# Kernel optimization log

Measured on AMD Instinct MI355X. Metric: run time of the kernel, lower is better.

## Reference

```python
import jax, jax.numpy as jnp
import numpy as np

N, F, H, C = 2048, 64, 64, 8

def setup_inputs() -> dict:
    key = jax.random.key(0)
    ks = jax.random.split(key, 8)
    s = 0.05  # small init like xavier gain=0.01
    return {
        "x": jax.random.normal(ks[0], (N, F), jnp.float32),
        "node_distances": jax.random.uniform(ks[1], (N, N), jnp.float32),
        "normalization_matrix": jnp.ones((N, N), jnp.float32),
        "W1": jax.random.normal(ks[2], (F, H), jnp.float32) * s,
        "b1": jnp.zeros((F, H), jnp.float32),
        "W2": jax.random.normal(ks[3], (F, H, C), jnp.float32) * s,
        "b2": jnp.zeros((F, C), jnp.float32),
        "Wm1": jax.random.normal(ks[4], (H,), jnp.float32) * s,
        "bm1": jnp.zeros((H,), jnp.float32),
        "Wm2": jax.random.normal(ks[5], (H,), jnp.float32) * s,
        "bm2": jnp.zeros((), jnp.float32),
    }

def reference(x, node_distances, normalization_matrix, W1, b1, W2, b2, Wm1, bm1, Wm2, bm2):
    # Per-feature NAM MLPs, vectorized over all F features (input dim is 1).
    # h[n,f,:] = relu(x[n,f] * W1[f] + b1[f])
    h = jax.nn.relu(x[:, :, None] * W1[None, :, :] + b1[None, :, :])        # [N,F,H]
    fx = jnp.einsum('nfh,fhc->nfc', h, W2) + b2[None, :, :]                 # [N,F,C]
    # Distance MLP m: Linear(1,H)->ReLU->Linear(H,1), limited_m => scalar weight per pair.
    d = node_distances / normalization_matrix                               # [N,N]
    hm = jax.nn.relu(d[:, :, None] * Wm1 + bm1)                             # [N,N,H]
    m = hm @ Wm2 + bm2                                                      # [N,N]
    # mf[c,i,f] = sum_j m[i,j]*fx[j,f,c]; out[c,i] = sum_f mf[c,i,f]
    # => out[i,c] = sum_j m[i,j] * (sum_f fx[j,f,c])  (identical math, fused)
    g = fx.sum(axis=1)                                                      # [N,C]
    out = m @ g                                                             # [N,C] == torch out.T
    return out
```

## Files before the change

kernel.cpp:

```cpp
#include <hip/hip_runtime.h>

#define NN 2048
#define FF 64
#define HH 64
#define CC 8
#define NB 2

#define INF __builtin_inff()

#define WS_T 0
#define WS_A 64
#define WS_B 129
#define WS_G 256

__global__ __launch_bounds__(256) void fused1_kernel(
    const float* __restrict__ x, const float* __restrict__ W1,
    const float* __restrict__ b1, const float* __restrict__ W2,
    const float* __restrict__ b2,
    const float* __restrict__ Wm1, const float* __restrict__ bm1,
    const float* __restrict__ Wm2, const float* __restrict__ bm2,
    float* __restrict__ ws)
{
    if (blockIdx.x == 256) {
        if (threadIdx.x >= 64) return;
        const int lane = threadIdx.x;

        float w  = Wm1[lane];
        float b  = bm1[lane];
        float m2 = Wm2[lane];
        float th = (w != 0.f) ? (-b / w) : INF;

        float v = th;
#pragma unroll
        for (int k = 2; k <= 64; k <<= 1) {
#pragma unroll
            for (int j = k >> 1; j >= 1; j >>= 1) {
                float o = __shfl_xor(v, j);
                bool up = ((lane & k) == 0);
                bool lower = ((lane & j) == 0);
                float mn = fminf(v, o), mx = fmaxf(v, o);
                v = (up == lower) ? mn : mx;
            }
        }
        ws[WS_T + lane] = v;

        float lo  = __shfl_up(v, 1);
        float hi  = v;
        float t63 = __shfl(v, 63);

        float dt;
        if (lane == 0) dt = (hi == INF) ? 0.f : hi - 1.f;
        else if (hi == INF) dt = (lo == INF) ? INF : lo + 1.f;
        else dt = 0.5f * (lo + hi);
        float dt64 = (t63 == INF) ? INF : t63 + 1.f;

        const float bm2v = bm2[0];
        float alpha = 0.f, beta = bm2v;
        float a64 = 0.f, b64 = bm2v;
#pragma unroll 8
        for (int h = 0; h < HH; ++h) {
            float wh = __shfl(w, h);
            float bh = __shfl(b, h);
            float mh = __shfl(m2, h);
            float tt = __shfl(th, h);
            bool act = (wh > 0.f) ? (dt > tt)
                     : ((wh < 0.f) ? (dt < tt) : (bh > 0.f));
            if (act) { alpha = fmaf(mh, wh, alpha); beta = fmaf(mh, bh, beta); }
            bool act64 = (wh > 0.f) ? (dt64 > tt)
                       : ((wh < 0.f) ? (dt64 < tt) : (bh > 0.f));
            if (act64) { a64 = fmaf(mh, wh, a64); b64 = fmaf(mh, bh, b64); }
        }
        ws[WS_A + lane] = alpha;
        ws[WS_B + lane] = beta;
        if (lane == 0) { ws[WS_A + 64] = a64; ws[WS_B + 64] = b64; }
        return;
    }

    float* g = ws + WS_G;
    const int wave = (blockIdx.x * 256 + threadIdx.x) >> 6;
    const int lane = threadIdx.x & 63;
    const int n0 = wave * NB;

    float xr[NB];
#pragma unroll
    for (int j = 0; j < NB; ++j) xr[j] = x[(n0 + j) * FF + lane];

    float acc[NB][CC];
#pragma unroll
    for (int j = 0; j < NB; ++j)
#pragma unroll
        for (int c = 0; c < CC; ++c) acc[j][c] = 0.f;

    float bs[CC];
    {
        const float4* bp = (const float4*)&b2[lane * CC];
        float4 a = bp[0], b = bp[1];
        bs[0] = a.x; bs[1] = a.y; bs[2] = a.z; bs[3] = a.w;
        bs[4] = b.x; bs[5] = b.y; bs[6] = b.z; bs[7] = b.w;
    }

#pragma unroll 4
    for (int f = 0; f < FF; ++f) {
        float w1 = W1[f * HH + lane];
        float bb = b1[f * HH + lane];
        const float4* w2p = (const float4*)&W2[(f * HH + lane) * CC];
        float4 wa = w2p[0];
        float4 wb = w2p[1];
#pragma unroll
        for (int j = 0; j < NB; ++j) {
            float xv = __shfl(xr[j], f);
            float hv = fmaxf(fmaf(xv, w1, bb), 0.f);
            acc[j][0] = fmaf(hv, wa.x, acc[j][0]);
            acc[j][1] = fmaf(hv, wa.y, acc[j][1]);
            acc[j][2] = fmaf(hv, wa.z, acc[j][2]);
            acc[j][3] = fmaf(hv, wa.w, acc[j][3]);
            acc[j][4] = fmaf(hv, wb.x, acc[j][4]);
            acc[j][5] = fmaf(hv, wb.y, acc[j][5]);
            acc[j][6] = fmaf(hv, wb.z, acc[j][6]);
            acc[j][7] = fmaf(hv, wb.w, acc[j][7]);
        }
    }

#pragma unroll
    for (int s = 32; s >= 1; s >>= 1) {
#pragma unroll
        for (int j = 0; j < NB; ++j)
#pragma unroll
            for (int c = 0; c < CC; ++c)
                acc[j][c] += __shfl_xor(acc[j][c], s);
#pragma unroll
        for (int c = 0; c < CC; ++c)
            bs[c] += __shfl_xor(bs[c], s);
    }

    if (lane == 0) {
#pragma unroll
        for (int j = 0; j < NB; ++j)
#pragma unroll
            for (int c = 0; c < CC; ++c)
                g[(n0 + j) * CC + c] = acc[j][c] + bs[c];
    }
}

__global__ __launch_bounds__(256) void out_kernel(
    const float* __restrict__ nd, const float* __restrict__ nm,
    const float* __restrict__ ws, const float* __restrict__ g,
    float* __restrict__ out)
{
    const int i = blockIdx.x;
    const int t = threadIdx.x;

    __shared__ float Tl[64], Al[65], Bl[65];
    if (t < 64) Tl[t] = ws[WS_T + t];
    else if (t < 129) Al[t - 64] = ws[WS_A + (t - 64)];
    else if (t < 194) Bl[t - 129] = ws[WS_B + (t - 129)];
    __syncthreads();

    const float4* nd4 = (const float4*)(nd + (size_t)i * NN);
    const float4* nm4 = (const float4*)(nm + (size_t)i * NN);
    float dv[8];
#pragma unroll
    for (int p = 0; p < 2; ++p) {
        float4 a = nd4[p * 256 + t];
        float4 b = nm4[p * 256 + t];
        float na[4] = {a.x, a.y, a.z, a.w};
        float nb[4] = {b.x, b.y, b.z, b.w};
#pragma unroll
        for (int e = 0; e < 4; ++e) {
            float r = __builtin_amdgcn_rcpf(nb[e]);
            r = r * fmaf(-nb[e], r, 2.0f);
            dv[p * 4 + e] = na[e] * r;
        }
    }

    float acc[CC];
#pragma unroll
    for (int c = 0; c < CC; ++c) acc[c] = 0.f;

#pragma unroll
    for (int p = 0; p < 2; ++p) {
#pragma unroll
        for (int e = 0; e < 4; ++e) {
            float d = dv[p * 4 + e];
            int lo = 0;
#pragma unroll
            for (int s = 32; s >= 1; s >>= 1)
                lo += (Tl[lo + s - 1] < d) ? s : 0;
            lo += (Tl[lo] < d) ? 1 : 0;
            float m = fmaf(d, Al[lo], Bl[lo]);

            int j = p * 1024 + t * 4 + e;
            const float4* gp = (const float4*)&g[j * CC];
            float4 ga = gp[0];
            float4 gb = gp[1];
            acc[0] = fmaf(m, ga.x, acc[0]);
            acc[1] = fmaf(m, ga.y, acc[1]);
            acc[2] = fmaf(m, ga.z, acc[2]);
            acc[3] = fmaf(m, ga.w, acc[3]);
            acc[4] = fmaf(m, gb.x, acc[4]);
            acc[5] = fmaf(m, gb.y, acc[5]);
            acc[6] = fmaf(m, gb.z, acc[6]);
            acc[7] = fmaf(m, gb.w, acc[7]);
        }
    }

#pragma unroll
    for (int s = 32; s >= 1; s >>= 1) {
#pragma unroll
        for (int c = 0; c < CC; ++c)
            acc[c] += __shfl_xor(acc[c], s);
    }

    __shared__ float red[4][CC];
    const int wv = t >> 6;
    const int lane = t & 63;
    if (lane == 0) {
#pragma unroll
        for (int c = 0; c < CC; ++c) red[wv][c] = acc[c];
    }
    __syncthreads();
    if (t < CC) {
        out[i * CC + t] = red[0][t] + red[1][t] + red[2][t] + red[3][t];
    }
}

extern "C" void kernel_launch(void* const* d_in, const int* in_sizes, int n_in,
                              void* d_out, int out_size, void* d_ws, size_t ws_size,
                              hipStream_t stream) {
    const float* x   = (const float*)d_in[0];
    const float* nd  = (const float*)d_in[1];
    const float* nm  = (const float*)d_in[2];
    const float* W1  = (const float*)d_in[3];
    const float* b1  = (const float*)d_in[4];
    const float* W2  = (const float*)d_in[5];
    const float* b2  = (const float*)d_in[6];
    const float* Wm1 = (const float*)d_in[7];
    const float* bm1 = (const float*)d_in[8];
    const float* Wm2 = (const float*)d_in[9];
    const float* bm2 = (const float*)d_in[10];
    float* out = (float*)d_out;
    float* ws  = (float*)d_ws;

    fused1_kernel<<<257, 256, 0, stream>>>(x, W1, b1, W2, b2,
                                           Wm1, bm1, Wm2, bm2, ws);
    out_kernel<<<NN, 256, 0, stream>>>(nd, nm, ws, ws + WS_G, out);
}
```

Baseline: 119.3 us.

## Fuse feature MLP and distance aggregation into one kernel with atomic accumulation

New measurement: 168.4 us. +41.1%, slower.

```diff
diff --git a/kernel.cpp b/kernel.cpp
--- a/kernel.cpp
+++ b/kernel.cpp
@@ -4,31 +4,105 @@
 #define FF 64
 #define HH 64
 #define CC 8
-#define NB 2
+
+#define CHUNK 32
+#define NCHUNK (NN / CHUNK)
+#define SPLIT 4
+#define ROWS (NN / SPLIT)
+#define NT 512
+#define NBW 4
 
 #define INF __builtin_inff()
 
-#define WS_T 0
-#define WS_A 64
-#define WS_B 129
-#define WS_G 256
-
-__global__ __launch_bounds__(256) void fused1_kernel(
-    const float* __restrict__ x, const float* __restrict__ W1,
-    const float* __restrict__ b1, const float* __restrict__ W2,
-    const float* __restrict__ b2,
+__global__ __launch_bounds__(NT) void fused_atomic(
+    const float* __restrict__ x,
+    const float* __restrict__ nd, const float* __restrict__ nm,
+    const float* __restrict__ W1, const float* __restrict__ b1,
+    const float* __restrict__ W2, const float* __restrict__ b2,
     const float* __restrict__ Wm1, const float* __restrict__ bm1,
     const float* __restrict__ Wm2, const float* __restrict__ bm2,
-    float* __restrict__ ws)
+    float* __restrict__ out)
 {
-    if (blockIdx.x == 256) {
-        if (threadIdx.x >= 64) return;
-        const int lane = threadIdx.x;
-
+    const int blk   = blockIdx.x;
+    const int chunk = blk >> 2;
+    const int rsp   = blk & 3;
+    const int j0    = chunk * CHUNK;
+    const int t     = threadIdx.x;
+    const int wv    = t >> 6;
+    const int lane  = t & 63;
+
+    __shared__ float gs[CHUNK][CC];
+    __shared__ float Tl[64], Al[65], Bl[65];
+
+    {
+        const int n0 = j0 + wv * NBW;
+
+        float xr[NBW];
+#pragma unroll
+        for (int j = 0; j < NBW; ++j) xr[j] = x[(n0 + j) * FF + lane];
+
+        float acc[NBW][CC];
+#pragma unroll
+        for (int j = 0; j < NBW; ++j)
+#pragma unroll
+            for (int c = 0; c < CC; ++c) acc[j][c] = 0.f;
+
+        float bs[CC];
+        {
+            const float4* bp = (const float4*)&b2[lane * CC];
+            float4 a = bp[0], bq = bp[1];
+            bs[0] = a.x; bs[1] = a.y; bs[2] = a.z; bs[3] = a.w;
+            bs[4] = bq.x; bs[5] = bq.y; bs[6] = bq.z; bs[7] = bq.w;
+        }
+
+#pragma unroll 4
+        for (int f = 0; f < FF; ++f) {
+            float w1 = W1[f * HH + lane];
+            float bb = b1[f * HH + lane];
+            const float4* w2p = (const float4*)&W2[(f * HH + lane) * CC];
+            float4 wa = w2p[0];
+            float4 wb = w2p[1];
+#pragma unroll
+            for (int j = 0; j < NBW; ++j) {
+                float xv = __shfl(xr[j], f);
+                float hv = fmaxf(fmaf(xv, w1, bb), 0.f);
+                acc[j][0] = fmaf(hv, wa.x, acc[j][0]);
+                acc[j][1] = fmaf(hv, wa.y, acc[j][1]);
+                acc[j][2] = fmaf(hv, wa.z, acc[j][2]);
+                acc[j][3] = fmaf(hv, wa.w, acc[j][3]);
+                acc[j][4] = fmaf(hv, wb.x, acc[j][4]);
+                acc[j][5] = fmaf(hv, wb.y, acc[j][5]);
+                acc[j][6] = fmaf(hv, wb.z, acc[j][6]);
+                acc[j][7] = fmaf(hv, wb.w, acc[j][7]);
+            }
+        }
+
+#pragma unroll
+        for (int s = 32; s >= 1; s >>= 1) {
+#pragma unroll
+            for (int j = 0; j < NBW; ++j)
+#pragma unroll
+                for (int c = 0; c < CC; ++c)
+                    acc[j][c] += __shfl_xor(acc[j][c], s);
+#pragma unroll
+            for (int c = 0; c < CC; ++c)
+                bs[c] += __shfl_xor(bs[c], s);
+        }
+
+        if (lane == 0) {
+#pragma unroll
+            for (int j = 0; j < NBW; ++j)
+#pragma unroll
+                for (int c = 0; c < CC; ++c)
+                    gs[wv * NBW + j][c] = acc[j][c] + bs[c];
+        }
+    }
+
+    if (wv == 0) {
         float w  = Wm1[lane];
-        float b  = bm1[lane];
+        float bb = bm1[lane];
         float m2 = Wm2[lane];
-        float th = (w != 0.f) ? (-b / w) : INF;
+        float th = (w != 0.f) ? (-bb / w) : INF;
 
         float v = th;
 #pragma unroll
@@ -42,7 +116,7 @@
                 v = (up == lower) ? mn : mx;
             }
         }
-        ws[WS_T + lane] = v;
+        Tl[lane] = v;
 
         float lo  = __shfl_up(v, 1);
         float hi  = v;
@@ -60,7 +134,7 @@
 #pragma unroll 8
         for (int h = 0; h < HH; ++h) {
             float wh = __shfl(w, h);
-            float bh = __shfl(b, h);
+            float bh = __shfl(bb, h);
             float mh = __shfl(m2, h);
             float tt = __shfl(th, h);
             bool act = (wh > 0.f) ? (dt > tt)
@@ -70,118 +144,34 @@
                        : ((wh < 0.f) ? (dt64 < tt) : (bh > 0.f));
             if (act64) { a64 = fmaf(mh, wh, a64); b64 = fmaf(mh, bh, b64); }
         }
-        ws[WS_A + lane] = alpha;
-        ws[WS_B + lane] = beta;
-        if (lane == 0) { ws[WS_A + 64] = a64; ws[WS_B + 64] = b64; }
-        return;
+        Al[lane] = alpha;
+        Bl[lane] = beta;
+        if (lane == 0) { Al[64] = a64; Bl[64] = b64; }
     }
 
-    float* g = ws + WS_G;
-    const int wave = (blockIdx.x * 256 + threadIdx.x) >> 6;
-    const int lane = threadIdx.x & 63;
-    const int n0 = wave * NB;
-
-    float xr[NB];
-#pragma unroll
-    for (int j = 0; j < NB; ++j) xr[j] = x[(n0 + j) * FF + lane];
-
-    float acc[NB][CC];
-#pragma unroll
-    for (int j = 0; j < NB; ++j)
-#pragma unroll
-        for (int c = 0; c < CC; ++c) acc[j][c] = 0.f;
-
-    float bs[CC];
-    {
-        const float4* bp = (const float4*)&b2[lane * CC];
-        float4 a = bp[0], b = bp[1];
-        bs[0] = a.x; bs[1] = a.y; bs[2] = a.z; bs[3] = a.w;
-        bs[4] = b.x; bs[5] = b.y; bs[6] = b.z; bs[7] = b.w;
-    }
-
-#pragma unroll 4
-    for (int f = 0; f < FF; ++f) {
-        float w1 = W1[f * HH + lane];
-        float bb = b1[f * HH + lane];
-        const float4* w2p = (const float4*)&W2[(f * HH + lane) * CC];
-        float4 wa = w2p[0];
-        float4 wb = w2p[1];
-#pragma unroll
-        for (int j = 0; j < NB; ++j) {
-            float xv = __shfl(xr[j], f);
-            float hv = fmaxf(fmaf(xv, w1, bb), 0.f);
-            acc[j][0] = fmaf(hv, wa.x, acc[j][0]);
-            acc[j][1] = fmaf(hv, wa.y, acc[j][1]);
-            acc[j][2] = fmaf(hv, wa.z, acc[j][2]);
-            acc[j][3] = fmaf(hv, wa.w, acc[j][3]);
-            acc[j][4] = fmaf(hv, wb.x, acc[j][4]);
-            acc[j][5] = fmaf(hv, wb.y, acc[j][5]);
-            acc[j][6] = fmaf(hv, wb.z, acc[j][6]);
-            acc[j][7] = fmaf(hv, wb.w, acc[j][7]);
-        }
-    }
-
-#pragma unroll
-    for (int s = 32; s >= 1; s >>= 1) {
-#pragma unroll
-        for (int j = 0; j < NB; ++j)
-#pragma unroll
-            for (int c = 0; c < CC; ++c)
-                acc[j][c] += __shfl_xor(acc[j][c], s);
-#pragma unroll
-        for (int c = 0; c < CC; ++c)
-            bs[c] += __shfl_xor(bs[c], s);
-    }
-
-    if (lane == 0) {
-#pragma unroll
-        for (int j = 0; j < NB; ++j)
-#pragma unroll
-            for (int c = 0; c < CC; ++c)
-                g[(n0 + j) * CC + c] = acc[j][c] + bs[c];
-    }
-}
-
-__global__ __launch_bounds__(256) void out_kernel(
-    const float* __restrict__ nd, const float* __restrict__ nm,
-    const float* __restrict__ ws, const float* __restrict__ g,
-    float* __restrict__ out)
-{
-    const int i = blockIdx.x;
-    const int t = threadIdx.x;
-
-    __shared__ float Tl[64], Al[65], Bl[65];
-    if (t < 64) Tl[t] = ws[WS_T + t];
-    else if (t < 129) Al[t - 64] = ws[WS_A + (t - 64)];
-    else if (t < 194) Bl[t - 129] = ws[WS_B + (t - 129)];
     __syncthreads();
 
-    const float4* nd4 = (const float4*)(nd + (size_t)i * NN);
-    const float4* nm4 = (const float4*)(nm + (size_t)i * NN);
-    float dv[8];
-#pragma unroll
-    for (int p = 0; p < 2; ++p) {
-        float4 a = nd4[p * 256 + t];
-        float4 b = nm4[p * 256 + t];
+    const int i = rsp * ROWS + t;
+
+    const float4* nd4 = (const float4*)(nd + (size_t)i * NN + j0);
+    const float4* nm4 = (const float4*)(nm + (size_t)i * NN + j0);
+
+    float acc[CC];
+#pragma unroll
+    for (int c = 0; c < CC; ++c) acc[c] = 0.f;
+
+#pragma unroll
+    for (int p = 0; p < CHUNK / 4; ++p) {
+        float4 a  = nd4[p];
+        float4 bq = nm4[p];
         float na[4] = {a.x, a.y, a.z, a.w};
-        float nb[4] = {b.x, b.y, b.z, b.w};
+        float nb[4] = {bq.x, bq.y, bq.z, bq.w};
 #pragma unroll
         for (int e = 0; e < 4; ++e) {
             float r = __builtin_amdgcn_rcpf(nb[e]);
             r = r * fmaf(-nb[e], r, 2.0f);
-            dv[p * 4 + e] = na[e] * r;
-        }
-    }
-
-    float acc[CC];
-#pragma unroll
-    for (int c = 0; c < CC; ++c) acc[c] = 0.f;
-
-#pragma unroll
-    for (int p = 0; p < 2; ++p) {
-#pragma unroll
-        for (int e = 0; e < 4; ++e) {
-            float d = dv[p * 4 + e];
+            float d = na[e] * r;
+
             int lo = 0;
 #pragma unroll
             for (int s = 32; s >= 1; s >>= 1)
@@ -189,8 +179,7 @@
             lo += (Tl[lo] < d) ? 1 : 0;
             float m = fmaf(d, Al[lo], Bl[lo]);
 
-            int j = p * 1024 + t * 4 + e;
-            const float4* gp = (const float4*)&g[j * CC];
+            const float4* gp = (const float4*)&gs[p * 4 + e][0];
             float4 ga = gp[0];
             float4 gb = gp[1];
             acc[0] = fmaf(m, ga.x, acc[0]);
@@ -205,23 +194,8 @@
     }
 
 #pragma unroll
-    for (int s = 32; s >= 1; s >>= 1) {
-#pragma unroll
-        for (int c = 0; c < CC; ++c)
-            acc[c] += __shfl_xor(acc[c], s);
-    }
-
-    __shared__ float red[4][CC];
-    const int wv = t >> 6;
-    const int lane = t & 63;
-    if (lane == 0) {
-#pragma unroll
-        for (int c = 0; c < CC; ++c) red[wv][c] = acc[c];
-    }
-    __syncthreads();
-    if (t < CC) {
-        out[i * CC + t] = red[0][t] + red[1][t] + red[2][t] + red[3][t];
-    }
+    for (int c = 0; c < CC; ++c)
+        atomicAdd(&out[i * CC + c], acc[c]);
 }
 
 extern "C" void kernel_launch(void* const* d_in, const int* in_sizes, int n_in,
@@ -239,9 +213,7 @@
     const float* Wm2 = (const float*)d_in[9];
     const float* bm2 = (const float*)d_in[10];
     float* out = (float*)d_out;
-    float* ws  = (float*)d_ws;
-
-    fused1_kernel<<<257, 256, 0, stream>>>(x, W1, b1, W2, b2,
-                                           Wm1, bm1, Wm2, bm2, ws);
-    out_kernel<<<NN, 256, 0, stream>>>(nd, nm, ws, ws + WS_G, out);
+
+    fused_atomic<<<NCHUNK * SPLIT, NT, 0, stream>>>(
+        x, nd, nm, W1, b1, W2, b2, Wm1, bm1, Wm2, bm2, out);
 }
```
